# Kernel tuning notes

Measured on AMD Instinct MI355X. Metric: run time of the kernel, lower is better.

## Reference

```python
import jax, jax.numpy as jnp
import numpy as np

NUM_HEADS = 16
EPS = 1e-6
NEG_INF = -1e9


def layer_norm(x, scale, bias):
    m = jnp.mean(x, axis=-1, keepdims=True)
    v = jnp.mean(jnp.square(x - m), axis=-1, keepdims=True)
    return (x - m) * jax.lax.rsqrt(v + EPS) * scale + bias


def mha(x_q, x_kv, wq, wk, wv, wo, causal):
    B, Sq, D = x_q.shape
    Sk = x_kv.shape[1]
    H = NUM_HEADS
    Dh = D // H
    q = (x_q @ wq).reshape(B, Sq, H, Dh) * (1.0 / np.sqrt(Dh))
    k = (x_kv @ wk).reshape(B, Sk, H, Dh)
    v = (x_kv @ wv).reshape(B, Sk, H, Dh)
    scores = jnp.einsum('bqhf,bkhf->bhqk', q, k)  # [B,H,Sq,Sk]
    if causal:
        mask = jnp.tril(jnp.ones((Sq, Sk), dtype=bool))
        scores = jnp.where(mask, scores, NEG_INF)
    p = jax.nn.softmax(scores, axis=-1)
    o = jnp.einsum('bhqk,bkhf->bqhf', p, v).reshape(B, Sq, D)
    return o @ wo


def setup_inputs() -> dict:
    key = jax.random.key(0)
    ks = jax.random.split(key, 12)
    B, S, D, F = 2, 2048, 1024, 4096
    w = 0.02
    return {
        'targets': jax.random.normal(ks[0], (B, S, D), jnp.float32),
        'encoded': jax.random.normal(ks[1], (B, S, D), jnp.float32),
        'ln1_s': jnp.ones((D,), jnp.float32),
        'ln1_b': jnp.zeros((D,), jnp.float32),
        'sa_wq': jax.random.normal(ks[2], (D, D), jnp.float32) * w,
        'sa_wk': jax.random.normal(ks[3], (D, D), jnp.float32) * w,
        'sa_wv': jax.random.normal(ks[4], (D, D), jnp.float32) * w,
        'sa_wo': jax.random.normal(ks[5], (D, D), jnp.float32) * w,
        'ln2_s': jnp.ones((D,), jnp.float32),
        'ln2_b': jnp.zeros((D,), jnp.float32),
        'ca_wq': jax.random.normal(ks[6], (D, D), jnp.float32) * w,
        'ca_wk': jax.random.normal(ks[7], (D, D), jnp.float32) * w,
        'ca_wv': jax.random.normal(ks[8], (D, D), jnp.float32) * w,
        'ca_wo': jax.random.normal(ks[9], (D, D), jnp.float32) * w,
        'ln3_s': jnp.ones((D,), jnp.float32),
        'ln3_b': jnp.zeros((D,), jnp.float32),
        'mlp_w1': jax.random.normal(ks[10], (D, F), jnp.float32) * w,
        'mlp_b1': jnp.zeros((F,), jnp.float32),
        'mlp_w2': jax.random.normal(ks[11], (F, D), jnp.float32) * w,
        'mlp_b2': jnp.zeros((D,), jnp.float32),
    }


def reference(targets, encoded, ln1_s, ln1_b, sa_wq, sa_wk, sa_wv, sa_wo,
              ln2_s, ln2_b, ca_wq, ca_wk, ca_wv, ca_wo,
              ln3_s, ln3_b, mlp_w1, mlp_b1, mlp_w2, mlp_b2):
    # Pre-LN causal self-attention + residual
    x = layer_norm(targets, ln1_s, ln1_b)
    x = mha(x, x, sa_wq, sa_wk, sa_wv, sa_wo, causal=True)
    x = x + targets
    # Pre-LN cross-attention over encoder output + residual
    y = layer_norm(x, ln2_s, ln2_b)
    y = mha(y, encoded, ca_wq, ca_wk, ca_wv, ca_wo, causal=False)
    y = y + x
    # Pre-LN MLP + residual
    z = layer_norm(y, ln3_s, ln3_b)
    z = jax.nn.relu(z @ mlp_w1 + mlp_b1) @ mlp_w2 + mlp_b2
    return y + z
```

## Files before the change

kernel.cpp:

```cpp
#include <hip/hip_runtime.h>


#define DEV __device__ __forceinline__

typedef __attribute__((ext_vector_type(8))) _Float16 half8;
typedef __attribute__((ext_vector_type(4))) _Float16 half4;
typedef __attribute__((ext_vector_type(2))) _Float16 half2v;
typedef __attribute__((ext_vector_type(4))) float    f32x4;

#define GLB(p) ((const __attribute__((address_space(1))) void*)(p))
#define LDS(p) ((__attribute__((address_space(3))) void*)(p))

DEV half2v pk(float a, float b) {
  return __builtin_bit_cast(half2v, __builtin_amdgcn_cvt_pkrtz(a, b));
}
DEV half4 pk4(float a, float b, float c, float d) {
  half2v lo = pk(a, b), hi = pk(c, d);
  half4 r; r.x = lo.x; r.y = lo.y; r.z = hi.x; r.w = hi.y;
  return r;
}

DEV float wave_sum_f(float v) {
  #pragma unroll
  for (int off = 32; off; off >>= 1) v += __shfl_xor(v, off);
  return v;
}

struct WtArgs { const float* w[8]; _Float16* wt[8]; };

__global__ __launch_bounds__(256) void wt_square(WtArgs a) {
  const float* w = a.w[blockIdx.z];
  _Float16* wt = a.wt[blockIdx.z];
  __shared__ float t[32][33];
  const int tx = threadIdx.x, ty = threadIdx.y;
  const int n0 = blockIdx.x * 32, k0 = blockIdx.y * 32;
  #pragma unroll
  for (int i = ty; i < 32; i += 8)
    t[i][tx] = w[(size_t)(k0 + i) * 1024 + n0 + tx];
  __syncthreads();
  #pragma unroll
  for (int i = ty; i < 32; i += 8)
    wt[(size_t)(n0 + i) * 1024 + k0 + tx] = (_Float16)t[tx][i];
}

__global__ __launch_bounds__(256) void wt_one(const float* __restrict__ w,
                                              _Float16* __restrict__ wt,
                                              int K, int N) {
  __shared__ float t[32][33];
  const int tx = threadIdx.x, ty = threadIdx.y;
  const int n0 = blockIdx.x * 32, k0 = blockIdx.y * 32;
  #pragma unroll
  for (int i = ty; i < 32; i += 8)
    t[i][tx] = w[(size_t)(k0 + i) * N + n0 + tx];
  __syncthreads();
  #pragma unroll
  for (int i = ty; i < 32; i += 8)
    wt[(size_t)(n0 + i) * K + k0 + tx] = (_Float16)t[tx][i];
}

__global__ __launch_bounds__(256) void cvt_f16(const float* __restrict__ in,
                                               _Float16* __restrict__ out) {
  const size_t i = ((size_t)blockIdx.x * 256 + threadIdx.x) * 4;
  const float4 v = *(const float4*)(in + i);
  *(half4*)(out + i) = pk4(v.x, v.y, v.z, v.w);
}

__global__ __launch_bounds__(256) void ln_kernel(const float* __restrict__ x,
                                                 const float* __restrict__ sc,
                                                 const float* __restrict__ bi,
                                                 _Float16* __restrict__ out) {
  const int row = blockIdx.x;
  const int t = threadIdx.x;
  const float4 v = ((const float4*)(x + (size_t)row * 1024))[t];
  float s  = v.x + v.y + v.z + v.w;
  float s2 = v.x * v.x + v.y * v.y + v.z * v.z + v.w * v.w;
  s = wave_sum_f(s); s2 = wave_sum_f(s2);
  __shared__ float red[8];
  const int lane = t & 63, wid = t >> 6;
  if (lane == 0) { red[wid] = s; red[4 + wid] = s2; }
  __syncthreads();
  s  = red[0] + red[1] + red[2] + red[3];
  s2 = red[4] + red[5] + red[6] + red[7];
  const float mean = s * (1.f / 1024.f);
  const float rstd = rsqrtf(s2 * (1.f / 1024.f) - mean * mean + 1e-6f);
  const float4 sv = ((const float4*)sc)[t];
  const float4 bv = ((const float4*)bi)[t];
  half4 o = pk4((v.x - mean) * rstd * sv.x + bv.x,
                (v.y - mean) * rstd * sv.y + bv.y,
                (v.z - mean) * rstd * sv.z + bv.z,
                (v.w - mean) * rstd * sv.w + bv.w);
  ((half4*)(out + (size_t)row * 1024))[t] = o;
}

template <int EPI, int BM, int BN>
__global__ __launch_bounds__(256)
void gemm_f16(const _Float16* __restrict__ A, const _Float16* __restrict__ Bt,
              void* __restrict__ Cout, const float* __restrict__ bias,
              const float* __restrict__ resid, int M, int N, int K,
              float scl, int sclCols, _Float16* __restrict__ vt, int vcol0) {
  constexpr int BK = 64;
  constexpr int AM = BM / 32;
  constexpr int AN = BN / 32;
  __shared__ _Float16 As[BM * BK];
  __shared__ _Float16 Bs[BN * BK];
  const int tid = threadIdx.x;
  const int lane = tid & 63, wid = tid >> 6;
  const int wm = wid >> 1, wn = wid & 1;
  const int q = lane >> 4, m15 = lane & 15;
  const int bm = blockIdx.y, bn = blockIdx.x;

  const _Float16* Ab = A + (size_t)bm * BM * K + (size_t)(tid >> 3) * K + (tid & 7) * 8;
  const _Float16* Bb = Bt + (size_t)bn * BN * K + (size_t)(tid >> 3) * K + (tid & 7) * 8;

  f32x4 acc[AM][AN] = {};

  for (int k0 = 0; k0 < K; k0 += BK) {
    if (k0) __syncthreads();
    #pragma unroll
    for (int r = 0; r < BM / 32; r++)
      __builtin_amdgcn_global_load_lds(GLB(Ab + (size_t)r * 32 * K + k0),
                                       LDS(&As[r * 2048 + wid * 512]), 16, 0, 0);
    #pragma unroll
    for (int r = 0; r < BN / 32; r++)
      __builtin_amdgcn_global_load_lds(GLB(Bb + (size_t)r * 32 * K + k0),
                                       LDS(&Bs[r * 2048 + wid * 512]), 16, 0, 0);
    __syncthreads();
    #pragma unroll
    for (int kk = 0; kk < 2; kk++) {
      half8 af[AM], bf[AN];
      #pragma unroll
      for (int i = 0; i < AM; i++)
        af[i] = *(const half8*)&As[(wm * (BM / 2) + i * 16 + m15) * BK + kk * 32 + q * 8];
      #pragma unroll
      for (int i = 0; i < AN; i++)
        bf[i] = *(const half8*)&Bs[(wn * (BN / 2) + i * 16 + m15) * BK + kk * 32 + q * 8];
      #pragma unroll
      for (int mi = 0; mi < AM; mi++)
        #pragma unroll
        for (int ni = 0; ni < AN; ni++)
          acc[mi][ni] = __builtin_amdgcn_mfma_f32_16x16x32_f16(af[mi], bf[ni],
                                                               acc[mi][ni], 0, 0, 0);
    }
  }

  const int rowbase = bm * BM + wm * (BM / 2);
  const int colbase = bn * BN + wn * (BN / 2);
  #pragma unroll
  for (int ni = 0; ni < AN; ni++) {
    const int col = colbase + ni * 16 + m15;
    float bv = 0.f;
    if (EPI == 2 || EPI == 4) bv = bias[col];
    const float cs = (EPI == 1 || EPI == 5) ? (col < sclCols ? scl : 1.f) : 1.f;
    if (EPI == 5 && col >= vcol0) {
      const int d = col & 63, hh = (col >> 6) & 15;
      #pragma unroll
      for (int mi = 0; mi < AM; mi++) {
        const int row = rowbase + mi * 16 + q * 4;
        const int bb = row >> 11, ss = row & 2047;
        half4 ov = pk4(acc[mi][ni][0], acc[mi][ni][1],
                       acc[mi][ni][2], acc[mi][ni][3]);
        *(half4*)(vt + ((size_t)(bb * 16 + hh) * 64 + d) * 2048 + ss) = ov;
      }
      continue;
    }
    #pragma unroll
    for (int mi = 0; mi < AM; mi++) {
      #pragma unroll
      for (int r = 0; r < 4; r++) {
        const int row = rowbase + mi * 16 + q * 4 + r;
        const size_t idx = (size_t)row * N + col;
        float v = acc[mi][ni][r];
        if (EPI == 1 || EPI == 5) {
          ((_Float16*)Cout)[idx] = (_Float16)(v * cs);
        } else if (EPI == 2) {
          v += bv; v = v > 0.f ? v : 0.f;
          ((_Float16*)Cout)[idx] = (_Float16)v;
        } else if (EPI == 3) {
          ((float*)Cout)[idx] = v + resid[idx];
        } else {
          ((float*)Cout)[idx] = v + bv + resid[idx];
        }
      }
    }
  }
}

__global__ __launch_bounds__(128)
void flash_attn(const _Float16* __restrict__ Q, int qs,
                const _Float16* __restrict__ Kp, int ks,
                const _Float16* __restrict__ Vt, _Float16* __restrict__ O,
                int S, int Sk, int causal) {
  __shared__ _Float16 Ks[64 * 72];
  __shared__ _Float16 Vs[64 * 72];
  __shared__ _Float16 Pq[2][32 * 72];
  const int tid = threadIdx.x;
  const int lane = tid & 63, wid = tid >> 6;
  const int quad = lane >> 4, c15 = lane & 15;
  const int h = blockIdx.y, b = blockIdx.z;
  int qb = blockIdx.x;
  if (causal) qb = (qb & 1) ? ((int)gridDim.x - 1 - (qb >> 1)) : (qb >> 1);
  const int qw0 = qb * 64 + wid * 32;

  half8 qf[2][2];
  #pragma unroll
  for (int nt = 0; nt < 2; nt++)
    #pragma unroll
    for (int kk = 0; kk < 2; kk++)
      qf[nt][kk] = *(const half8*)(Q + (size_t)(b * S + qw0 + nt * 16 + c15) * qs +
                                   h * 64 + kk * 32 + quad * 8);

  f32x4 oacc[4][2];
  #pragma unroll
  for (int i = 0; i < 4; i++)
    #pragma unroll
    for (int j = 0; j < 2; j++)
      oacc[i][j] = (f32x4){0.f, 0.f, 0.f, 0.f};
  float lpart[2] = {0.f, 0.f};

  const int ntiles = causal ? (qb + 1) : (Sk >> 6);
  const _Float16* Kg = Kp + (size_t)b * Sk * ks + h * 64;
  const _Float16* Vg = Vt + (size_t)(b * 16 + h) * 64 * Sk;

  const int srow = tid >> 3, sg8 = (tid & 7) * 8;
  half8 rk[4], rv[4];
  auto ldkv = [&](int jb) {
    #pragma unroll
    for (int i = 0; i < 4; i++) {
      rk[i] = *(const half8*)(Kg + (size_t)(jb + srow + i * 16) * ks + sg8);
      rv[i] = *(const half8*)(Vg + (size_t)(srow + i * 16) * Sk + jb + sg8);
    }
  };
  ldkv(0);

  for (int t = 0; t < ntiles; t++) {
    const int jb = t * 64;
    __syncthreads();
    #pragma unroll
    for (int i = 0; i < 4; i++) {
      *(half8*)&Ks[(srow + i * 16) * 72 + sg8] = rk[i];
      *(half8*)&Vs[(srow + i * 16) * 72 + sg8] = rv[i];
    }
    __syncthreads();
    if (t + 1 < ntiles) ldkv(jb + 64);

    f32x4 s[4][2];
    #pragma unroll
    for (int mt = 0; mt < 4; mt++) {
      const half8 kf0 = *(const half8*)&Ks[(mt * 16 + c15) * 72 + quad * 8];
      const half8 kf1 = *(const half8*)&Ks[(mt * 16 + c15) * 72 + 32 + quad * 8];
      #pragma unroll
      for (int nt = 0; nt < 2; nt++) {
        f32x4 z = {0.f, 0.f, 0.f, 0.f};
        z = __builtin_amdgcn_mfma_f32_16x16x32_f16(kf0, qf[nt][0], z, 0, 0, 0);
        z = __builtin_amdgcn_mfma_f32_16x16x32_f16(kf1, qf[nt][1], z, 0, 0, 0);
        s[mt][nt] = z;
      }
    }

    if (causal && jb + 63 > qw0) {
      #pragma unroll
      for (int mt = 0; mt < 4; mt++)
        #pragma unroll
        for (int nt = 0; nt < 2; nt++) {
          const int qglob = qw0 + nt * 16 + c15;
          #pragma unroll
          for (int rr = 0; rr < 4; rr++) {
            const int kglob = jb + mt * 16 + quad * 4 + rr;
            if (kglob > qglob) s[mt][nt][rr] = -1e30f;
          }
        }
    }

    #pragma unroll
    for (int nt = 0; nt < 2; nt++) {
      float psum = 0.f;
      #pragma unroll
      for (int mt = 0; mt < 4; mt++) {
        #pragma unroll
        for (int rr = 0; rr < 4; rr++) {
          const float p = exp2f(s[mt][nt][rr]);
          s[mt][nt][rr] = p;
          psum += p;
        }
      }
      lpart[nt] += psum;
      #pragma unroll
      for (int mtk = 0; mtk < 4; mtk++) {
        *(half4*)&Pq[wid][(nt * 16 + c15) * 72 + mtk * 16 + quad * 4] =
            pk4(s[mtk][nt][0], s[mtk][nt][1], s[mtk][nt][2], s[mtk][nt][3]);
      }
    }

    half8 pb[2][2];
    #pragma unroll
    for (int kk = 0; kk < 2; kk++)
      #pragma unroll
      for (int nt = 0; nt < 2; nt++)
        pb[kk][nt] = *(const half8*)&Pq[wid][(nt * 16 + c15) * 72 + kk * 32 + quad * 8];
    #pragma unroll
    for (int mtd = 0; mtd < 4; mtd++) {
      const half8 vf0 = *(const half8*)&Vs[(mtd * 16 + c15) * 72 + quad * 8];
      const half8 vf1 = *(const half8*)&Vs[(mtd * 16 + c15) * 72 + 32 + quad * 8];
      #pragma unroll
      for (int nt = 0; nt < 2; nt++) {
        oacc[mtd][nt] = __builtin_amdgcn_mfma_f32_16x16x32_f16(vf0, pb[0][nt],
                                                               oacc[mtd][nt], 0, 0, 0);
        oacc[mtd][nt] = __builtin_amdgcn_mfma_f32_16x16x32_f16(vf1, pb[1][nt],
                                                               oacc[mtd][nt], 0, 0, 0);
      }
    }
  }

  #pragma unroll
  for (int nt = 0; nt < 2; nt++) {
    float l = lpart[nt];
    l += __shfl_xor(l, 16);
    l += __shfl_xor(l, 32);
    const float linv = 1.f / l;
    #pragma unroll
    for (int mtd = 0; mtd < 4; mtd++) {
      half4 ov = pk4(oacc[mtd][nt][0] * linv, oacc[mtd][nt][1] * linv,
                     oacc[mtd][nt][2] * linv, oacc[mtd][nt][3] * linv);
      *(half4*)(O + (size_t)(b * S + qw0 + nt * 16 + c15) * 1024 +
                h * 64 + mtd * 16 + quad * 4) = ov;
    }
  }
}

extern "C" void kernel_launch(void* const* d_in, const int* in_sizes, int n_in,
                              void* d_out, int out_size, void* d_ws, size_t ws_size,
                              hipStream_t stream) {
  const float* targets = (const float*)d_in[0];
  const float* encoded = (const float*)d_in[1];
  const float* ln1_s = (const float*)d_in[2];
  const float* ln1_b = (const float*)d_in[3];
  const float* sa_wq = (const float*)d_in[4];
  const float* sa_wk = (const float*)d_in[5];
  const float* sa_wv = (const float*)d_in[6];
  const float* sa_wo = (const float*)d_in[7];
  const float* ln2_s = (const float*)d_in[8];
  const float* ln2_b = (const float*)d_in[9];
  const float* ca_wq = (const float*)d_in[10];
  const float* ca_wk = (const float*)d_in[11];
  const float* ca_wv = (const float*)d_in[12];
  const float* ca_wo = (const float*)d_in[13];
  const float* ln3_s = (const float*)d_in[14];
  const float* ln3_b = (const float*)d_in[15];
  const float* mlp_w1 = (const float*)d_in[16];
  const float* mlp_b1 = (const float*)d_in[17];
  const float* mlp_w2 = (const float*)d_in[18];
  const float* mlp_b2 = (const float*)d_in[19];

  const int B = 2, S = 2048, D = 1024, F = 4096, M = B * S;
  const size_t MB = 1024ull * 1024ull;
  const float QSCALE = 0.125f * 1.44269504f;
  char* ws = (char*)d_ws;
  _Float16* wsq   = (_Float16*)(ws);
  _Float16* w1t   = (_Float16*)(ws + 16 * MB);
  _Float16* w2t   = (_Float16*)(ws + 24 * MB);
  _Float16* Abf   = (_Float16*)(ws + 32 * MB);
  _Float16* encbf = (_Float16*)(ws + 40 * MB);
  _Float16* QKV   = (_Float16*)(ws + 48 * MB);
  _Float16* Qcb   = (_Float16*)(ws + 48 * MB);
  _Float16* KVb   = (_Float16*)(ws + 56 * MB);
  _Float16* h1    = (_Float16*)(ws + 48 * MB);
  _Float16* Vtb   = (_Float16*)(ws + 80 * MB);
  _Float16* Aob   = (_Float16*)(ws + 88 * MB);
  float*    xres  = (float*)(ws + 96 * MB);
  float*    yres  = (float*)(ws + 112 * MB);

  {
    WtArgs wa;
    const float* sw[8] = {sa_wq, sa_wk, sa_wv, sa_wo, ca_wq, ca_wk, ca_wv, ca_wo};
    for (int i = 0; i < 8; i++) { wa.w[i] = sw[i]; wa.wt[i] = wsq + (size_t)i * D * D; }
    wt_square<<<dim3(32, 32, 8), dim3(32, 8), 0, stream>>>(wa);
  }
  wt_one<<<dim3(F / 32, D / 32), dim3(32, 8), 0, stream>>>(mlp_w1, w1t, D, F);
  wt_one<<<dim3(D / 32, F / 32), dim3(32, 8), 0, stream>>>(mlp_w2, w2t, F, D);
  cvt_f16<<<(M * D) / 1024, 256, 0, stream>>>(encoded, encbf);

  const dim3 gA(S / 64, 16, B);

  ln_kernel<<<M, 256, 0, stream>>>(targets, ln1_s, ln1_b, Abf);
  gemm_f16<5, 128, 128><<<dim3(3072 / 128, M / 128), 256, 0, stream>>>(
      Abf, wsq, QKV, nullptr, nullptr, M, 3072, D, QSCALE, 1024, Vtb, 2048);
  flash_attn<<<gA, 128, 0, stream>>>(QKV, 3072, QKV + 1024, 3072, Vtb, Aob, S, S, 1);
  gemm_f16<3, 128, 64><<<dim3(1024 / 64, M / 128), 256, 0, stream>>>(
      Aob, wsq + 3ull * D * D, xres, nullptr, targets, M, D, D, 1.f, 0, nullptr, 0);

  ln_kernel<<<M, 256, 0, stream>>>(xres, ln2_s, ln2_b, Abf);
  gemm_f16<1, 128, 64><<<dim3(1024 / 64, M / 128), 256, 0, stream>>>(
      Abf, wsq + 4ull * D * D, Qcb, nullptr, nullptr, M, D, D, QSCALE, 1024, nullptr, 0);
  gemm_f16<5, 128, 128><<<dim3(2048 / 128, M / 128), 256, 0, stream>>>(
      encbf, wsq + 5ull * D * D, KVb, nullptr, nullptr, M, 2048, D, 1.f, 0, Vtb, 1024);
  flash_attn<<<gA, 128, 0, stream>>>(Qcb, 1024, KVb, 2048, Vtb, Aob, S, S, 0);
  gemm_f16<3, 128, 64><<<dim3(1024 / 64, M / 128), 256, 0, stream>>>(
      Aob, wsq + 7ull * D * D, yres, nullptr, xres, M, D, D, 1.f, 0, nullptr, 0);

  ln_kernel<<<M, 256, 0, stream>>>(yres, ln3_s, ln3_b, Abf);
  gemm_f16<2, 128, 128><<<dim3(F / 128, M / 128), 256, 0, stream>>>(
      Abf, w1t, h1, mlp_b1, nullptr, M, F, D, 1.f, 0, nullptr, 0);
  gemm_f16<4, 128, 64><<<dim3(1024 / 64, M / 128), 256, 0, stream>>>(
      h1, w2t, (float*)d_out, mlp_b2, yres, M, D, F, 1.f, 0, nullptr, 0);

  (void)in_sizes; (void)n_in; (void)out_size; (void)ws_size;
}
```

Measured before the change: 594.0 us.

## Double-buffer GEMM shared-memory tiles and retune tile sizes per GEMM

```diff
diff --git a/kernel.cpp b/kernel.cpp
--- a/kernel.cpp
+++ b/kernel.cpp
@@ -92,48 +92,59 @@
   ((half4*)(out + (size_t)row * 1024))[t] = o;
 }
 
-template <int EPI, int BM, int BN>
+template <int EPI, int BM, int BN, int BK>
 __global__ __launch_bounds__(256)
 void gemm_f16(const _Float16* __restrict__ A, const _Float16* __restrict__ Bt,
               void* __restrict__ Cout, const float* __restrict__ bias,
               const float* __restrict__ resid, int M, int N, int K,
               float scl, int sclCols, _Float16* __restrict__ vt, int vcol0) {
-  constexpr int BK = 64;
   constexpr int AM = BM / 32;
   constexpr int AN = BN / 32;
-  __shared__ _Float16 As[BM * BK];
-  __shared__ _Float16 Bs[BN * BK];
+  constexpr int RA = BM * BK / 2048;
+  constexpr int RB = BN * BK / 2048;
+  constexpr int TPR = BK / 8;
+  constexpr int RPR = 2048 / BK;
+  __shared__ _Float16 As[2][BM * BK];
+  __shared__ _Float16 Bs[2][BN * BK];
   const int tid = threadIdx.x;
   const int lane = tid & 63, wid = tid >> 6;
   const int wm = wid >> 1, wn = wid & 1;
   const int q = lane >> 4, m15 = lane & 15;
   const int bm = blockIdx.y, bn = blockIdx.x;
 
-  const _Float16* Ab = A + (size_t)bm * BM * K + (size_t)(tid >> 3) * K + (tid & 7) * 8;
-  const _Float16* Bb = Bt + (size_t)bn * BN * K + (size_t)(tid >> 3) * K + (tid & 7) * 8;
+  const int trow = tid / TPR;
+  const int tcol = (tid % TPR) * 8;
+  const _Float16* Ab = A + ((size_t)bm * BM + trow) * K + tcol;
+  const _Float16* Bb = Bt + ((size_t)bn * BN + trow) * K + tcol;
 
   f32x4 acc[AM][AN] = {};
 
-  for (int k0 = 0; k0 < K; k0 += BK) {
-    if (k0) __syncthreads();
-    #pragma unroll
-    for (int r = 0; r < BM / 32; r++)
-      __builtin_amdgcn_global_load_lds(GLB(Ab + (size_t)r * 32 * K + k0),
-                                       LDS(&As[r * 2048 + wid * 512]), 16, 0, 0);
-    #pragma unroll
-    for (int r = 0; r < BN / 32; r++)
-      __builtin_amdgcn_global_load_lds(GLB(Bb + (size_t)r * 32 * K + k0),
-                                       LDS(&Bs[r * 2048 + wid * 512]), 16, 0, 0);
+  auto stage = [&](int k0, int buf) {
+    #pragma unroll
+    for (int r = 0; r < RA; r++)
+      __builtin_amdgcn_global_load_lds(GLB(Ab + (size_t)r * RPR * K + k0),
+                                       LDS(&As[buf][r * 2048 + wid * 512]), 16, 0, 0);
+    #pragma unroll
+    for (int r = 0; r < RB; r++)
+      __builtin_amdgcn_global_load_lds(GLB(Bb + (size_t)r * RPR * K + k0),
+                                       LDS(&Bs[buf][r * 2048 + wid * 512]), 16, 0, 0);
+  };
+
+  stage(0, 0);
+  const int nit = K / BK;
+  for (int it = 0; it < nit; it++) {
+    const int buf = it & 1;
     __syncthreads();
-    #pragma unroll
-    for (int kk = 0; kk < 2; kk++) {
+    if (it + 1 < nit) stage((it + 1) * BK, buf ^ 1);
+    #pragma unroll
+    for (int kk = 0; kk < BK / 32; kk++) {
       half8 af[AM], bf[AN];
       #pragma unroll
       for (int i = 0; i < AM; i++)
-        af[i] = *(const half8*)&As[(wm * (BM / 2) + i * 16 + m15) * BK + kk * 32 + q * 8];
+        af[i] = *(const half8*)&As[buf][(wm * (BM / 2) + i * 16 + m15) * BK + kk * 32 + q * 8];
       #pragma unroll
       for (int i = 0; i < AN; i++)
-        bf[i] = *(const half8*)&Bs[(wn * (BN / 2) + i * 16 + m15) * BK + kk * 32 + q * 8];
+        bf[i] = *(const half8*)&Bs[buf][(wn * (BN / 2) + i * 16 + m15) * BK + kk * 32 + q * 8];
       #pragma unroll
       for (int mi = 0; mi < AM; mi++)
         #pragma unroll
@@ -382,25 +393,25 @@
   const dim3 gA(S / 64, 16, B);
 
   ln_kernel<<<M, 256, 0, stream>>>(targets, ln1_s, ln1_b, Abf);
-  gemm_f16<5, 128, 128><<<dim3(3072 / 128, M / 128), 256, 0, stream>>>(
+  gemm_f16<5, 128, 128, 32><<<dim3(3072 / 128, M / 128), 256, 0, stream>>>(
       Abf, wsq, QKV, nullptr, nullptr, M, 3072, D, QSCALE, 1024, Vtb, 2048);
   flash_attn<<<gA, 128, 0, stream>>>(QKV, 3072, QKV + 1024, 3072, Vtb, Aob, S, S, 1);
-  gemm_f16<3, 128, 64><<<dim3(1024 / 64, M / 128), 256, 0, stream>>>(
+  gemm_f16<3, 64, 64, 64><<<dim3(1024 / 64, M / 64), 256, 0, stream>>>(
       Aob, wsq + 3ull * D * D, xres, nullptr, targets, M, D, D, 1.f, 0, nullptr, 0);
 
   ln_kernel<<<M, 256, 0, stream>>>(xres, ln2_s, ln2_b, Abf);
-  gemm_f16<1, 128, 64><<<dim3(1024 / 64, M / 128), 256, 0, stream>>>(
+  gemm_f16<1, 64, 64, 64><<<dim3(1024 / 64, M / 64), 256, 0, stream>>>(
       Abf, wsq + 4ull * D * D, Qcb, nullptr, nullptr, M, D, D, QSCALE, 1024, nullptr, 0);
-  gemm_f16<5, 128, 128><<<dim3(2048 / 128, M / 128), 256, 0, stream>>>(
+  gemm_f16<5, 64, 128, 32><<<dim3(2048 / 128, M / 64), 256, 0, stream>>>(
       encbf, wsq + 5ull * D * D, KVb, nullptr, nullptr, M, 2048, D, 1.f, 0, Vtb, 1024);
   flash_attn<<<gA, 128, 0, stream>>>(Qcb, 1024, KVb, 2048, Vtb, Aob, S, S, 0);
-  gemm_f16<3, 128, 64><<<dim3(1024 / 64, M / 128), 256, 0, stream>>>(
+  gemm_f16<3, 64, 64, 64><<<dim3(1024 / 64, M / 64), 256, 0, stream>>>(
       Aob, wsq + 7ull * D * D, yres, nullptr, xres, M, D, D, 1.f, 0, nullptr, 0);
 
   ln_kernel<<<M, 256, 0, stream>>>(yres, ln3_s, ln3_b, Abf);
-  gemm_f16<2, 128, 128><<<dim3(F / 128, M / 128), 256, 0, stream>>>(
+  gemm_f16<2, 128, 128, 32><<<dim3(F / 128, M / 128), 256, 0, stream>>>(
       Abf, w1t, h1, mlp_b1, nullptr, M, F, D, 1.f, 0, nullptr, 0);
-  gemm_f16<4, 128, 64><<<dim3(1024 / 64, M / 128), 256, 0, stream>>>(
+  gemm_f16<4, 64, 64, 64><<<dim3(1024 / 64, M / 64), 256, 0, stream>>>(
       h1, w2t, (float*)d_out, mlp_b2, yres, M, D, F, 1.f, 0, nullptr, 0);
 
   (void)in_sizes; (void)n_in; (void)out_size; (void)ws_size;
```

New measurement: 589.2 us. No clear change (-0.8%).
